# Kernel tuning notes

Hardware: AMD Instinct MI355X
Metric: run time of the kernel (lower is better)

## Reference

```python
import jax, jax.numpy as jnp
import numpy as np

B, N, S, CIN, COUT, GDIM = 4, 128, 8, 8, 8, 7  # batch, points, coset samples, channels, g_embed+2*q_embed


def setup_inputs() -> dict:
    key = jax.random.key(0)
    ks = jax.random.split(key, 8)
    pairwise_g = jax.random.normal(ks[0], (B, N, N, S, S, GDIM), jnp.float32)
    coset_functions = jax.random.normal(ks[1], (B, N, S, CIN), jnp.float32)
    mask = jax.random.bernoulli(ks[2], 0.9, (B, N, S))  # bool key mask (B,N,S)
    # per-channel SumKernel params: k_y = Linear(2->1), k_g = Linear(GDIM->1), stacked over CIN channels
    w_y = jax.random.normal(ks[3], (CIN, 2), jnp.float32) * 0.1
    b_y = jax.random.normal(ks[4], (CIN,), jnp.float32) * 0.1
    w_g = jax.random.normal(ks[5], (CIN, GDIM), jnp.float32) * 0.1
    b_g = jax.random.normal(ks[6], (CIN,), jnp.float32) * 0.1
    w_lin = jax.random.normal(ks[7], (COUT, CIN), jnp.float32) * (1.0 / np.sqrt(CIN))
    return {"pairwise_g": pairwise_g, "coset_functions": coset_functions, "mask": mask,
            "w_y": w_y, "b_y": b_y, "w_g": w_g, "b_g": b_g, "w_lin": w_lin}


def reference(pairwise_g, coset_functions, mask, w_y, b_y, w_g, b_g, w_lin):
    # Vectorized over the original per-channel Python loop: channel axis c.
    y = coset_functions  # (B, N, S, C)
    # k_g(pairwise_g) per channel + both biases: (B,i,j,s1,s2,C)
    logits = jnp.einsum('bijstg,cg->bijstc', pairwise_g, w_g) + (b_g + b_y)
    # k_y([y_1, y_2]): y_1 indexed by key (j, s2) -> weight w_y[:,0]; y_2 by query (i, s1) -> w_y[:,1]
    key_term = y * w_y[:, 0]   # (B, N, S, C)
    qry_term = y * w_y[:, 1]   # (B, N, S, C)
    logits = logits + key_term[:, None, :, None, :, :] + qry_term[:, :, None, :, None, :]
    # plain exp (original does NOT subtract a max), zero out masked keys (j, s2)
    att = jnp.where(mask[:, None, :, None, :, None], jnp.exp(logits), 0.0)
    att = att / att.sum(axis=(2, 4), keepdims=True)  # normalize over key dims
    # weighted sum of key values over (j, s2), residual add
    out = y + jnp.einsum('bijstc,bjtc->bisc', att, y)
    out = out * mask[..., None].astype(out.dtype)
    # output linear c_in -> c_out, no bias (torch Linear: x @ W.T)
    return out @ w_lin.T
```

## Files before the change

### kernel.cpp

```cpp
#include <hip/hip_runtime.h>


namespace {

constexpr int kN = 128, kS = 8, kC = 8, kO = 8, kG = 7;
constexpr int JSTRIDE = 68;

__global__ __launch_bounds__(256, 2)
void emha_kernel(const float* __restrict__ pg,
                 const float* __restrict__ y,
                 const int*   __restrict__ mask,
                 const float* __restrict__ w_y,
                 const float* __restrict__ w_g,
                 const float* __restrict__ w_lin,
                 float*       __restrict__ out)
{
    __shared__ float lds_kw[kN * JSTRIDE];
    __shared__ float lds_kv[kN * JSTRIDE];
    __shared__ float red[4][8][16];
    __shared__ float obuf[8][8];

    const int t  = threadIdx.x;
    const int bi = blockIdx.x;
    const int b  = bi >> 7;
    const int i  = bi & 127;

    const float* pbase = pg + (size_t)bi * (kN * kS * kS * kG) + (size_t)t * 56;

    float4 buf[2][7];
    {
        const float4* s0 = reinterpret_cast<const float4*>(pbase);
#pragma unroll
        for (int q = 0; q < 7; ++q) buf[0][q] = s0[q];
    }

    float wg[kC][kG];
#pragma unroll
    for (int c = 0; c < kC; ++c)
#pragma unroll
        for (int g = 0; g < kG; ++g)
            wg[c][g] = w_g[c * kG + g];

    const float* yb = y    + b * (kN * kS * kC);
    const int*   mb = mask + b * (kN * kS);
    const float  wy0 = w_y[2 * (t & 7)];
#pragma unroll
    for (int k = 0; k < 32; ++k) {
        const int idx = t + k * 256;
        const float yv = yb[idx];
        const int   m  = mb[idx >> 3];
        const float kw = m ? __expf(yv * wy0) : 0.0f;
        const int off = (idx >> 6) * JSTRIDE + (idx & 63);
        lds_kw[off] = kw;
        lds_kv[off] = kw * yv;
    }
    __syncthreads();

    const int jl = t >> 3;
    float num[kC], den[kC];
#pragma unroll
    for (int c = 0; c < kC; ++c) { num[c] = 0.0f; den[c] = 0.0f; }

#pragma unroll
    for (int h = 0; h < 8; ++h) {
        if (h < 7) {
            const int hn = h + 1;
            const float4* sn = reinterpret_cast<const float4*>(
                pbase + (hn >> 1) * 14336 + (hn & 1) * 28);
#pragma unroll
            for (int q = 0; q < 7; ++q) buf[hn & 1][q] = sn[q];
        }

        const float* p = reinterpret_cast<const float*>(buf[h & 1]);
        const int j = (h >> 1) * 32 + jl;
#pragma unroll
        for (int s2i = 0; s2i < 4; ++s2i) {
            const int s2 = (h & 1) * 4 + s2i;
            const int lo = j * JSTRIDE + s2 * 8;
            const float4 kva = *reinterpret_cast<const float4*>(&lds_kv[lo]);
            const float4 kvb = *reinterpret_cast<const float4*>(&lds_kv[lo + 4]);
            const float4 kwa = *reinterpret_cast<const float4*>(&lds_kw[lo]);
            const float4 kwb = *reinterpret_cast<const float4*>(&lds_kw[lo + 4]);
            const float kv[8] = {kva.x, kva.y, kva.z, kva.w, kvb.x, kvb.y, kvb.z, kvb.w};
            const float kw[8] = {kwa.x, kwa.y, kwa.z, kwa.w, kwb.x, kwb.y, kwb.z, kwb.w};
#pragma unroll
            for (int c = 0; c < kC; ++c) {
                float d =      p[s2i * kG + 0] * wg[c][0];
                d = fmaf(p[s2i * kG + 1], wg[c][1], d);
                d = fmaf(p[s2i * kG + 2], wg[c][2], d);
                d = fmaf(p[s2i * kG + 3], wg[c][3], d);
                d = fmaf(p[s2i * kG + 4], wg[c][4], d);
                d = fmaf(p[s2i * kG + 5], wg[c][5], d);
                d = fmaf(p[s2i * kG + 6], wg[c][6], d);
                const float e = __expf(d);
                num[c] = fmaf(e, kv[c], num[c]);
                den[c] = fmaf(e, kw[c], den[c]);
            }
        }
    }

#pragma unroll
    for (int c = 0; c < kC; ++c) {
        num[c] += __shfl_xor(num[c], 8);
        num[c] += __shfl_xor(num[c], 16);
        num[c] += __shfl_xor(num[c], 32);
        den[c] += __shfl_xor(den[c], 8);
        den[c] += __shfl_xor(den[c], 16);
        den[c] += __shfl_xor(den[c], 32);
    }
    const int wave = t >> 6;
    const int lane = t & 63;
    if (lane < 8) {
#pragma unroll
        for (int c = 0; c < kC; ++c) {
            red[wave][lane][c]     = num[c];
            red[wave][lane][c + 8] = den[c];
        }
    }
    __syncthreads();

    if (t < 64) {
        const int s1q = t >> 3, c = t & 7;
        float ns = 0.0f, ds = 0.0f;
#pragma unroll
        for (int w = 0; w < 4; ++w) { ns += red[w][s1q][c]; ds += red[w][s1q][c + 8]; }
        const float yv = yb[(i * kS + s1q) * kC + c];
        const int   m  = mb[i * kS + s1q];
        obuf[s1q][c] = m ? (yv + ns / ds) : 0.0f;
    }
    __syncthreads();

    if (t < 64) {
        const int s1q = t >> 3, o = t & 7;
        float acc = 0.0f;
#pragma unroll
        for (int c = 0; c < kC; ++c)
            acc = fmaf(obuf[s1q][c], w_lin[o * kC + c], acc);
        out[(size_t)bi * (kS * kO) + t] = acc;
    }
}

}

extern "C" void kernel_launch(void* const* d_in, const int* in_sizes, int n_in,
                              void* d_out, int out_size, void* d_ws, size_t ws_size,
                              hipStream_t stream)
{
    const float* pg    = (const float*)d_in[0];
    const float* y     = (const float*)d_in[1];
    const int*   mask  = (const int*)  d_in[2];
    const float* w_y   = (const float*)d_in[3];
    const float* w_g   = (const float*)d_in[5];
    const float* w_lin = (const float*)d_in[7];
    float* out = (float*)d_out;

    emha_kernel<<<4 * kN, 256, 0, stream>>>(pg, y, mask, w_y, w_g, w_lin, out);
}
```

Measured before the change: 32.50 us.

## Stream pairwise_g through LDS with async global_load_lds double buffering

Replaces the per-thread register double buffer of pairwise_g with chunked direct global-to-LDS loads (global_load_lds), double-buffered across eight chunks and ordered with manual vmcnt waits. The thread-to-(j,s2) mapping and the shuffle reduction pattern change to match the new LDS layout, where each wave reads only the region it loaded itself. The goal is to hide global latency and avoid register staging. The cost is a large LDS footprint, so launch bounds drop to one block per CU, which reduces occupancy.

```diff
diff --git a/kernel.cpp b/kernel.cpp
--- a/kernel.cpp
+++ b/kernel.cpp
@@ -5,8 +5,14 @@
 
 constexpr int kN = 128, kS = 8, kC = 8, kO = 8, kG = 7;
 constexpr int JSTRIDE = 68;
+constexpr int CH_PAIRS  = 128;
+constexpr int CH_FLOATS = CH_PAIRS * 56;
+constexpr int NCH = 8;
 
-__global__ __launch_bounds__(256, 2)
+typedef const __attribute__((address_space(1))) unsigned int* gp_t;
+typedef __attribute__((address_space(3))) unsigned int* lp_t;
+
+__global__ __launch_bounds__(256, 1)
 void emha_kernel(const float* __restrict__ pg,
                  const float* __restrict__ y,
                  const int*   __restrict__ mask,
@@ -15,23 +21,28 @@
                  const float* __restrict__ w_lin,
                  float*       __restrict__ out)
 {
+    __shared__ float pay[2][CH_FLOATS];
     __shared__ float lds_kw[kN * JSTRIDE];
     __shared__ float lds_kv[kN * JSTRIDE];
     __shared__ float red[4][8][16];
     __shared__ float obuf[8][8];
 
-    const int t  = threadIdx.x;
-    const int bi = blockIdx.x;
-    const int b  = bi >> 7;
-    const int i  = bi & 127;
+    const int t    = threadIdx.x;
+    const int bi   = blockIdx.x;
+    const int b    = bi >> 7;
+    const int i    = bi & 127;
+    const int w    = t >> 6;
+    const int lane = t & 63;
 
-    const float* pbase = pg + (size_t)bi * (kN * kS * kS * kG) + (size_t)t * 56;
+    const float* slab = pg + (size_t)bi * (kN * kS * kS * kG);
 
-    float4 buf[2][7];
     {
-        const float4* s0 = reinterpret_cast<const float4*>(pbase);
+        const float* gs = slab + w * 1792 + lane * 4;
 #pragma unroll
-        for (int q = 0; q < 7; ++q) buf[0][q] = s0[q];
+        for (int q = 0; q < 7; ++q)
+            __builtin_amdgcn_global_load_lds((gp_t)(gs + q * 256),
+                                             (lp_t)(&pay[0][w * 1792 + q * 256]),
+                                             16, 0, 0);
     }
 
     float wg[kC][kG];
@@ -49,34 +60,46 @@
         const int idx = t + k * 256;
         const float yv = yb[idx];
         const int   m  = mb[idx >> 3];
-        const float kw = m ? __expf(yv * wy0) : 0.0f;
+        const float kwv = m ? __expf(yv * wy0) : 0.0f;
         const int off = (idx >> 6) * JSTRIDE + (idx & 63);
-        lds_kw[off] = kw;
-        lds_kv[off] = kw * yv;
+        lds_kw[off] = kwv;
+        lds_kv[off] = kwv * yv;
     }
-    __syncthreads();
+    asm volatile("s_waitcnt lgkmcnt(0)" ::: "memory");
+    __builtin_amdgcn_s_barrier();
 
-    const int jl = t >> 3;
+    const int m  = t >> 1;
+    const int h  = t & 1;
     float num[kC], den[kC];
 #pragma unroll
     for (int c = 0; c < kC; ++c) { num[c] = 0.0f; den[c] = 0.0f; }
 
 #pragma unroll
-    for (int h = 0; h < 8; ++h) {
-        if (h < 7) {
-            const int hn = h + 1;
-            const float4* sn = reinterpret_cast<const float4*>(
-                pbase + (hn >> 1) * 14336 + (hn & 1) * 28);
+    for (int c = 0; c < NCH; ++c) {
+        if (c + 1 < NCH) {
+            const float* gs = slab + (c + 1) * CH_FLOATS + w * 1792 + lane * 4;
+            float* db = pay[(c + 1) & 1];
 #pragma unroll
-            for (int q = 0; q < 7; ++q) buf[hn & 1][q] = sn[q];
+            for (int q = 0; q < 7; ++q)
+                __builtin_amdgcn_global_load_lds((gp_t)(gs + q * 256),
+                                                 (lp_t)(db + w * 1792 + q * 256),
+                                                 16, 0, 0);
+            asm volatile("s_waitcnt vmcnt(7)" ::: "memory");
+        } else {
+            asm volatile("s_waitcnt vmcnt(0)" ::: "memory");
         }
 
-        const float* p = reinterpret_cast<const float*>(buf[h & 1]);
-        const int j = (h >> 1) * 32 + jl;
+        const float* p = &pay[c & 1][m * 56 + h * 28];
+        float4 qv[7];
+#pragma unroll
+        for (int q = 0; q < 7; ++q)
+            qv[q] = reinterpret_cast<const float4*>(p)[q];
+        const float* pf = reinterpret_cast<const float*>(qv);
+
+        const int j = 16 * c + (m >> 3);
 #pragma unroll
         for (int s2i = 0; s2i < 4; ++s2i) {
-            const int s2 = (h & 1) * 4 + s2i;
-            const int lo = j * JSTRIDE + s2 * 8;
+            const int lo = j * JSTRIDE + (h * 4 + s2i) * 8;
             const float4 kva = *reinterpret_cast<const float4*>(&lds_kv[lo]);
             const float4 kvb = *reinterpret_cast<const float4*>(&lds_kv[lo + 4]);
             const float4 kwa = *reinterpret_cast<const float4*>(&lds_kw[lo]);
@@ -84,49 +107,48 @@
             const float kv[8] = {kva.x, kva.y, kva.z, kva.w, kvb.x, kvb.y, kvb.z, kvb.w};
             const float kw[8] = {kwa.x, kwa.y, kwa.z, kwa.w, kwb.x, kwb.y, kwb.z, kwb.w};
 #pragma unroll
-            for (int c = 0; c < kC; ++c) {
-                float d =      p[s2i * kG + 0] * wg[c][0];
-                d = fmaf(p[s2i * kG + 1], wg[c][1], d);
-                d = fmaf(p[s2i * kG + 2], wg[c][2], d);
-                d = fmaf(p[s2i * kG + 3], wg[c][3], d);
-                d = fmaf(p[s2i * kG + 4], wg[c][4], d);
-                d = fmaf(p[s2i * kG + 5], wg[c][5], d);
-                d = fmaf(p[s2i * kG + 6], wg[c][6], d);
+            for (int cc = 0; cc < kC; ++cc) {
+                float d =      pf[s2i * kG + 0] * wg[cc][0];
+                d = fmaf(pf[s2i * kG + 1], wg[cc][1], d);
+                d = fmaf(pf[s2i * kG + 2], wg[cc][2], d);
+                d = fmaf(pf[s2i * kG + 3], wg[cc][3], d);
+                d = fmaf(pf[s2i * kG + 4], wg[cc][4], d);
+                d = fmaf(pf[s2i * kG + 5], wg[cc][5], d);
+                d = fmaf(pf[s2i * kG + 6], wg[cc][6], d);
                 const float e = __expf(d);
-                num[c] = fmaf(e, kv[c], num[c]);
-                den[c] = fmaf(e, kw[c], den[c]);
+                num[cc] = fmaf(e, kv[cc], num[cc]);
+                den[cc] = fmaf(e, kw[cc], den[cc]);
             }
         }
     }
 
 #pragma unroll
     for (int c = 0; c < kC; ++c) {
-        num[c] += __shfl_xor(num[c], 8);
+        num[c] += __shfl_xor(num[c], 1);
         num[c] += __shfl_xor(num[c], 16);
         num[c] += __shfl_xor(num[c], 32);
-        den[c] += __shfl_xor(den[c], 8);
+        den[c] += __shfl_xor(den[c], 1);
         den[c] += __shfl_xor(den[c], 16);
         den[c] += __shfl_xor(den[c], 32);
     }
-    const int wave = t >> 6;
-    const int lane = t & 63;
-    if (lane < 8) {
+    if (lane < 16 && (lane & 1) == 0) {
+        const int s1 = lane >> 1;
 #pragma unroll
         for (int c = 0; c < kC; ++c) {
-            red[wave][lane][c]     = num[c];
-            red[wave][lane][c + 8] = den[c];
+            red[w][s1][c]     = num[c];
+            red[w][s1][c + 8] = den[c];
         }
     }
     __syncthreads();
 
     if (t < 64) {
-        const int s1q = t >> 3, c = t & 7;
+        const int s1q = t >> 3, cc = t & 7;
         float ns = 0.0f, ds = 0.0f;
 #pragma unroll
-        for (int w = 0; w < 4; ++w) { ns += red[w][s1q][c]; ds += red[w][s1q][c + 8]; }
-        const float yv = yb[(i * kS + s1q) * kC + c];
-        const int   m  = mb[i * kS + s1q];
-        obuf[s1q][c] = m ? (yv + ns / ds) : 0.0f;
+        for (int ww = 0; ww < 4; ++ww) { ns += red[ww][s1q][cc]; ds += red[ww][s1q][cc + 8]; }
+        const float yv = yb[(i * kS + s1q) * kC + cc];
+        const int   mq = mb[i * kS + s1q];
+        obuf[s1q][cc] = mq ? (yv + ns / ds) : 0.0f;
     }
     __syncthreads();
 
```

After: 36.51 us. +12.3%, slower.
